# Kernel tuning notes

Measured on AMD Instinct MI355X. Metric: run time of the kernel, lower is better.

## Reference

```python
import jax, jax.numpy as jnp
import numpy as np

B, T, D = 64, 4096, 512

def setup_inputs() -> dict:
    key = jax.random.key(0)
    k1, k2 = jax.random.split(key)
    x = jax.random.normal(k1, (B, T, D), dtype=jnp.float32)
    W = jax.random.normal(k2, (D, 1), dtype=jnp.float32)
    b = jnp.zeros((T, 1), dtype=jnp.float32)
    return {"x": x, "W": W, "b": b}

def reference(x, W, b):
    # e: [B, T, 1] = tanh(x @ W + b), b broadcast over batch
    e = jnp.tanh(jnp.einsum('btd,do->bto', x, W) + b)
    a = jax.nn.softmax(e, axis=1)          # softmax over time axis
    return jnp.sum(a * x, axis=1)          # [B, D]
```

## Files before the change

### kernel.cpp

```cpp
#include <hip/hip_runtime.h>
#include <math.h>

#define Bsz 64
#define Tsz 4096
#define Dsz 512
#define ROWS 32
#define THREADS 512
#define CHUNKS (Tsz / ROWS)

__global__ __launch_bounds__(THREADS) void attn_phase1(
    const float* __restrict__ x, const float* __restrict__ W,
    const float* __restrict__ bias, float* __restrict__ num,
    float* __restrict__ den) {
  __shared__ float xs[ROWS * Dsz];
  __shared__ float wrow[ROWS];

  const int tid  = threadIdx.x;
  const int lane = tid & 63;
  const int wave = tid >> 6;
  const int s = blockIdx.x;
  const int b = blockIdx.y;

  const float* src = x + ((size_t)b * Tsz + (size_t)s * ROWS) * Dsz;

  float Wreg[8];
#pragma unroll
  for (int k = 0; k < 8; ++k) Wreg[k] = W[lane + 64 * k];

  {
    const float4* s4 = (const float4*)src;
    float4* l4 = (float4*)xs;
#pragma unroll
    for (int it = 0; it < 8; ++it)
      l4[it * THREADS + tid] = s4[it * THREADS + tid];
  }
  __syncthreads();

#pragma unroll
  for (int q = 0; q < 4; ++q) {
    const int r = wave + 8 * q;
    const float* xr = xs + r * Dsz;
    float p = 0.f;
#pragma unroll
    for (int k = 0; k < 8; ++k) p += xr[lane + 64 * k] * Wreg[k];
#pragma unroll
    for (int off = 32; off >= 1; off >>= 1) p += __shfl_xor(p, off, 64);
    if (lane == 0) {
      float e = tanhf(p + bias[s * ROWS + r]);
      wrow[r] = expf(e);
    }
  }
  __syncthreads();

  if (wave == 0) {
    float dv = (lane < ROWS) ? wrow[lane] : 0.f;
#pragma unroll
    for (int off = 32; off >= 1; off >>= 1) dv += __shfl_xor(dv, off, 64);
    if (lane == 0) atomicAdd(&den[b], dv);
  }

  float acc = 0.f;
#pragma unroll
  for (int t = 0; t < ROWS; ++t) acc += wrow[t] * xs[t * Dsz + tid];
  atomicAdd(&num[(size_t)b * Dsz + tid], acc);
}

__global__ __launch_bounds__(512) void attn_phase2(
    const float* __restrict__ num, const float* __restrict__ den,
    float* __restrict__ out) {
  const int i = blockIdx.x * blockDim.x + threadIdx.x;
  const int b = i >> 9;
  out[i] = num[i] / den[b];
}

extern "C" void kernel_launch(void* const* d_in, const int* in_sizes, int n_in,
                              void* d_out, int out_size, void* d_ws, size_t ws_size,
                              hipStream_t stream) {
  const float* x    = (const float*)d_in[0];
  const float* W    = (const float*)d_in[1];
  const float* bias = (const float*)d_in[2];
  float* num = (float*)d_ws;
  float* den = num + (size_t)Bsz * Dsz;

  hipMemsetAsync(d_ws, 0, ((size_t)Bsz * Dsz + Bsz) * sizeof(float), stream);

  dim3 g1(CHUNKS, Bsz);
  attn_phase1<<<g1, THREADS, 0, stream>>>(x, W, bias, num, den);
  attn_phase2<<<Bsz, Dsz, 0, stream>>>(num, den, (float*)d_out);
}
```

Measured before the change: 691.4 us.

## Make phase1 persistent over time slices with double-buffered register prefetch

Each block now walks 512 time rows in chunks of 16, prefetching the next chunk into registers while computing the current one from a double-buffered shared tile. Partial sums for the numerator and denominator stay in registers and are written with one atomic per block rather than one per 32-row chunk, which cuts the atomic count. The grid shrinks from 8192 blocks to 512 (8 slices by 64 batches) at 4 blocks per CU, which may leave the 256 CUs underoccupied, and the loop adds two barriers per chunk.

```diff
diff --git a/kernel.cpp b/kernel.cpp
--- a/kernel.cpp
+++ b/kernel.cpp
@@ -4,65 +4,88 @@
 #define Bsz 64
 #define Tsz 4096
 #define Dsz 512
-#define ROWS 32
+#define SLICES 8
+#define CH 16
+#define ITERS (Tsz / SLICES / CH)
 #define THREADS 512
-#define CHUNKS (Tsz / ROWS)
 
-__global__ __launch_bounds__(THREADS) void attn_phase1(
+__global__ __launch_bounds__(THREADS, 4) void attn_phase1(
     const float* __restrict__ x, const float* __restrict__ W,
     const float* __restrict__ bias, float* __restrict__ num,
     float* __restrict__ den) {
-  __shared__ float xs[ROWS * Dsz];
-  __shared__ float wrow[ROWS];
+  __shared__ float xs[2][CH * Dsz];
+  __shared__ float wts[2][CH];
 
   const int tid  = threadIdx.x;
   const int lane = tid & 63;
   const int wave = tid >> 6;
-  const int s = blockIdx.x;
-  const int b = blockIdx.y;
+  const int sb = blockIdx.x;
+  const int b  = blockIdx.y;
+  const int row0 = sb * (Tsz / SLICES);
 
-  const float* src = x + ((size_t)b * Tsz + (size_t)s * ROWS) * Dsz;
+  const float* src = x + ((size_t)b * Tsz + row0) * Dsz;
 
   float Wreg[8];
 #pragma unroll
   for (int k = 0; k < 8; ++k) Wreg[k] = W[lane + 64 * k];
 
+  float4 pf[4];
   {
     const float4* s4 = (const float4*)src;
-    float4* l4 = (float4*)xs;
 #pragma unroll
-    for (int it = 0; it < 8; ++it)
-      l4[it * THREADS + tid] = s4[it * THREADS + tid];
+    for (int i = 0; i < 4; ++i) pf[i] = s4[i * THREADS + tid];
+    float4* l4 = (float4*)xs[0];
+#pragma unroll
+    for (int i = 0; i < 4; ++i) l4[i * THREADS + tid] = pf[i];
   }
   __syncthreads();
 
+  float acc = 0.f;
+  float den_acc = 0.f;
+
+  for (int c = 0; c < ITERS; ++c) {
+    const int cur = c & 1, nxt = cur ^ 1;
+    const bool more = (c + 1 < ITERS);
+
+    if (more) {
+      const float4* n4 = (const float4*)(src + (size_t)(c + 1) * CH * Dsz);
 #pragma unroll
-  for (int q = 0; q < 4; ++q) {
-    const int r = wave + 8 * q;
-    const float* xr = xs + r * Dsz;
-    float p = 0.f;
+      for (int i = 0; i < 4; ++i) pf[i] = n4[i * THREADS + tid];
+    }
+
 #pragma unroll
-    for (int k = 0; k < 8; ++k) p += xr[lane + 64 * k] * Wreg[k];
+    for (int q = 0; q < 2; ++q) {
+      const int r = wave + 8 * q;
+      const float* xr = xs[cur] + r * Dsz;
+      float p = 0.f;
 #pragma unroll
-    for (int off = 32; off >= 1; off >>= 1) p += __shfl_xor(p, off, 64);
-    if (lane == 0) {
-      float e = tanhf(p + bias[s * ROWS + r]);
-      wrow[r] = expf(e);
+      for (int k = 0; k < 8; ++k) p += xr[lane + 64 * k] * Wreg[k];
+#pragma unroll
+      for (int off = 32; off >= 1; off >>= 1) p += __shfl_xor(p, off, 64);
+      if (lane == 0) wts[cur][r] = expf(tanhf(p + bias[row0 + c * CH + r]));
     }
-  }
-  __syncthreads();
+    __syncthreads();
 
-  if (wave == 0) {
-    float dv = (lane < ROWS) ? wrow[lane] : 0.f;
 #pragma unroll
-    for (int off = 32; off >= 1; off >>= 1) dv += __shfl_xor(dv, off, 64);
-    if (lane == 0) atomicAdd(&den[b], dv);
+    for (int t = 0; t < CH; ++t) acc += wts[cur][t] * xs[cur][t * Dsz + tid];
+
+    if (wave == 0) {
+      float dv = (lane < CH) ? wts[cur][lane] : 0.f;
+#pragma unroll
+      for (int off = 8; off >= 1; off >>= 1) dv += __shfl_xor(dv, off, 64);
+      den_acc += dv;
+    }
+
+    if (more) {
+      float4* n4l = (float4*)xs[nxt];
+#pragma unroll
+      for (int i = 0; i < 4; ++i) n4l[i * THREADS + tid] = pf[i];
+    }
+    __syncthreads();
   }
 
-  float acc = 0.f;
-#pragma unroll
-  for (int t = 0; t < ROWS; ++t) acc += wrow[t] * xs[t * Dsz + tid];
   atomicAdd(&num[(size_t)b * Dsz + tid], acc);
+  if (wave == 0 && lane == 0) atomicAdd(&den[b], den_acc);
 }
 
 __global__ __launch_bounds__(512) void attn_phase2(
@@ -84,7 +107,7 @@
 
   hipMemsetAsync(d_ws, 0, ((size_t)Bsz * Dsz + Bsz) * sizeof(float), stream);
 
-  dim3 g1(CHUNKS, Bsz);
+  dim3 g1(SLICES, Bsz);
   attn_phase1<<<g1, THREADS, 0, stream>>>(x, W, bias, num, den);
   attn_phase2<<<Bsz, Dsz, 0, stream>>>(num, den, (float*)d_out);
 }
```

Result: slower. 753.7 us (+9.0%).
